# Kernel optimization log

Measured on AMD Instinct MI355X. Metric: run time of the kernel, lower is better.

## Reference

```python
import jax, jax.numpy as jnp
import numpy as np

B, R, C, IC, OC = 32, 16384, 16, 16, 16  # batch, num_routes, num_capsules, in_ch, out_ch
NUM_ITERATIONS = 3


def squash(s, axis=-1):
    # scale * s / norm with scale = norm^2/(1+norm^2)  ==  norm/(1+norm^2) * s
    norm = jnp.linalg.norm(s, axis=axis, keepdims=True)
    return (norm / (1.0 + norm * norm)) * s


def setup_inputs() -> dict:
    key = jax.random.key(0)
    kx, kw = jax.random.split(key)
    x = jax.random.normal(kx, (B, C, IC), dtype=jnp.float32)
    # W param: torch shape (1, R, C, OC, IC); leading 1 squeezed here
    W = jax.random.normal(kw, (R, C, OC, IC), dtype=jnp.float32)
    return {"x": x, "W": W}


def reference(x, W):
    # u_hat[b,r,c,o] = sum_i W[r,c,o,i] * x[b,c,i]   (torch broadcast of x over routes)
    u_hat = jnp.einsum('rcoi,bci->brco', W, x)  # (B, R, C, OC)
    b = jnp.zeros((x.shape[0], R, C, 1), dtype=u_hat.dtype)
    outputs = None
    for it in range(NUM_ITERATIONS):
        c = jax.nn.softmax(b, axis=1)                      # softmax over routes
        s = (c * u_hat).sum(axis=1, keepdims=True)         # (B, 1, C, OC)
        outputs = squash(s)
        if it < NUM_ITERATIONS - 1:
            b = b + (u_hat * outputs).sum(axis=-1, keepdims=True)
    return outputs.squeeze(axis=1)  # (B, C, OC)
```

## Files before the change

### kernel.cpp

```cpp
#include <hip/hip_runtime.h>
#include <math.h>


typedef __attribute__((ext_vector_type(8)))  short short8;
typedef __attribute__((ext_vector_type(16))) float f32x16;

union FU { short8 s; unsigned int u[4]; };

typedef const __attribute__((address_space(1))) void GV;
typedef __attribute__((address_space(3))) void LV;

__device__ __forceinline__ void splitpk(float a, float b,
                                        unsigned int& hp, unsigned int& lp) {
    unsigned int ua = __float_as_uint(a), ub = __float_as_uint(b);
    unsigned int ta = ua + 0x7FFFu + ((ua >> 16) & 1u);
    unsigned int tb = ub + 0x7FFFu + ((ub >> 16) & 1u);
    hp = (ta >> 16) | (tb & 0xFFFF0000u);
    float ha = __uint_as_float(ta & 0xFFFF0000u);
    float hb = __uint_as_float(tb & 0xFFFF0000u);
    unsigned int la = __float_as_uint(a - ha) + 0x8000u;
    unsigned int lb = __float_as_uint(b - hb) + 0x8000u;
    lp = (la >> 16) | (lb & 0xFFFF0000u);
}

__global__ __launch_bounds__(256) void k_zero(float* __restrict__ ws) {
    ws[blockIdx.x * 256 + threadIdx.x] = 0.f;
}

__global__ __launch_bounds__(256) void k_wsum(const float4* __restrict__ W4,
                                              float* __restrict__ wsum) {
    int gid = blockIdx.x * 256 + threadIdx.x;
    float4 acc = {0.f, 0.f, 0.f, 0.f};
    int idx = gid;
    #pragma unroll
    for (int it = 0; it < 64; ++it) {
        float4 w = W4[idx];
        acc.x += w.x; acc.y += w.y; acc.z += w.z; acc.w += w.w;
        idx += 262144;
    }
    int cls = gid & 1023;
    atomicAdd(&wsum[cls * 4 + 0], acc.x);
    atomicAdd(&wsum[cls * 4 + 1], acc.y);
    atomicAdd(&wsum[cls * 4 + 2], acc.z);
    atomicAdd(&wsum[cls * 4 + 3], acc.w);
}

__global__ __launch_bounds__(256) void k_v1(const float* __restrict__ wsum,
                                            const float* __restrict__ x,
                                            float* __restrict__ v1) {
    int t = blockIdx.x * 256 + threadIdx.x;
    int o = t & 15, c = (t >> 4) & 15, b = t >> 8;
    const float* xb = x + (b * 16 + c) * 16;
    const float* wr = wsum + (c * 16 + o) * 16;
    float s = 0.f;
    #pragma unroll
    for (int i = 0; i < 16; ++i) s += wr[i] * xb[i];
    s *= (1.0f / 16384.0f);
    float ns = s * s;
    #pragma unroll
    for (int d = 1; d < 16; d <<= 1) ns += __shfl_xor(ns, d);
    v1[t] = s * (sqrtf(ns) / (1.0f + ns));
}

__global__ __launch_bounds__(256) void k_vout_vs(const float* __restrict__ E,
                                                 const float* __restrict__ Z,
                                                 const float* __restrict__ v1,
                                                 float* __restrict__ vs) {
    int t = blockIdx.x * 256 + threadIdx.x;
    float s = E[t] / Z[t >> 4];
    float ns = s * s;
    #pragma unroll
    for (int d = 1; d < 16; d <<= 1) ns += __shfl_xor(ns, d);
    vs[t] = v1[t] + s * (sqrtf(ns) / (1.0f + ns));
}

__global__ __launch_bounds__(256) void k_vout(const float* __restrict__ E,
                                              const float* __restrict__ Z,
                                              float* __restrict__ dst) {
    int t = blockIdx.x * 256 + threadIdx.x;
    float s = E[t] / Z[t >> 4];
    float ns = s * s;
    #pragma unroll
    for (int d = 1; d < 16; d <<= 1) ns += __shfl_xor(ns, d);
    dst[t] = s * (sqrtf(ns) / (1.0f + ns));
}

__global__ __launch_bounds__(512)
void k_iter(const float* __restrict__ W,
            const float* __restrict__ x,
            const float* __restrict__ v,
            float* __restrict__ E,
            float* __restrict__ Z) {
    __shared__ float4 Wr[4 * 1024];
    __shared__ float sV[512];
    __shared__ float E_lds[512];
    __shared__ float Z_lds[32];

    int c = blockIdx.y;
    int r0 = blockIdx.x * 256;
    int tid = threadIdx.x, wv = tid >> 6, l = tid & 63;
    int m  = l & 31;
    int hi = l >> 5;

    { int b = tid >> 4, o = tid & 15;
      sV[tid] = v[b * 256 + c * 16 + o];
      E_lds[tid] = 0.f; }
    if (tid < 32) Z_lds[tid] = 0.f;

    FU bh, bl;
    {
        const float4* xb = (const float4*)x + m * 64 + c * 4 + hi * 2;
        float4 x0 = xb[0], x1 = xb[1];
        splitpk(x0.x, x0.y, bh.u[0], bl.u[0]);
        splitpk(x0.z, x0.w, bh.u[1], bl.u[1]);
        splitpk(x1.x, x1.y, bh.u[2], bl.u[2]);
        splitpk(x1.z, x1.w, bh.u[3], bl.u[3]);
    }
    __syncthreads();

    float vf[16];
    #pragma unroll
    for (int reg = 0; reg < 16; ++reg) {
        int o = (reg & 3) + 4 * hi + 8 * ((reg >> 2) & 1);
        vf[reg] = sV[m * 16 + o];
    }

    float accE[16];
    #pragma unroll
    for (int reg = 0; reg < 16; ++reg) accE[reg] = 0.f;
    float accZ = 0.f;

    asm volatile("s_waitcnt vmcnt(0)" ::: "memory");

    const float4* W4c = (const float4*)W + (size_t)c * 64;

#define STAGE(sl, cn) {                                                        \
        const float4* s0 = W4c +                                               \
            (size_t)(r0 + (cn) * 16 + wv * 2 + (m >> 4)) * 1024 +              \
            (m & 15) * 4 + hi * 2;                                             \
        __builtin_amdgcn_global_load_lds((GV*)s0,                              \
            (LV*)&Wr[(sl) * 1024 + wv * 128], 16, 0, 0);                       \
        __builtin_amdgcn_global_load_lds((GV*)(s0 + 1),                        \
            (LV*)&Wr[(sl) * 1024 + wv * 128 + 64], 16, 0, 0);                  \
    }

    STAGE(0, 0); STAGE(1, 1); STAGE(2, 2);

    #pragma unroll
    for (int chunk = 0; chunk < 16; ++chunk) {
        if (chunk <= 12) STAGE((chunk + 3) & 3, chunk + 3);

        if (chunk <= 12)      asm volatile("s_waitcnt vmcnt(6)" ::: "memory");
        else if (chunk == 13) asm volatile("s_waitcnt vmcnt(4)" ::: "memory");
        else if (chunk == 14) asm volatile("s_waitcnt vmcnt(2)" ::: "memory");
        else                  asm volatile("s_waitcnt vmcnt(0)" ::: "memory");

        int sb = (chunk & 3) * 1024 + wv * 128 + l;
        float4 ca = Wr[sb];
        float4 cb = Wr[sb + 64];

        FU ah, al;
        splitpk(ca.x, ca.y, ah.u[0], al.u[0]);
        splitpk(ca.z, ca.w, ah.u[1], al.u[1]);
        splitpk(cb.x, cb.y, ah.u[2], al.u[2]);
        splitpk(cb.z, cb.w, ah.u[3], al.u[3]);

        f32x16 cf;
        #pragma unroll
        for (int i = 0; i < 16; ++i) cf[i] = 0.f;
        cf = __builtin_amdgcn_mfma_f32_32x32x16_bf16(al.s, bl.s, cf, 0, 0, 0);
        cf = __builtin_amdgcn_mfma_f32_32x32x16_bf16(ah.s, bl.s, cf, 0, 0, 0);
        cf = __builtin_amdgcn_mfma_f32_32x32x16_bf16(al.s, bh.s, cf, 0, 0, 0);
        cf = __builtin_amdgcn_mfma_f32_32x32x16_bf16(ah.s, bh.s, cf, 0, 0, 0);

        float Lp0 = 0.f, Lp1 = 0.f;
        #pragma unroll
        for (int reg = 0; reg < 8; ++reg)  Lp0 += cf[reg] * vf[reg];
        #pragma unroll
        for (int reg = 8; reg < 16; ++reg) Lp1 += cf[reg] * vf[reg];
        float Lv0 = Lp0 + __shfl_xor(Lp0, 32);
        float Lv1 = Lp1 + __shfl_xor(Lp1, 32);
        float e0 = __expf(Lv0), e1 = __expf(Lv1);
        accZ += e0 + e1;
        #pragma unroll
        for (int reg = 0; reg < 8; ++reg)  accE[reg] += e0 * cf[reg];
        #pragma unroll
        for (int reg = 8; reg < 16; ++reg) accE[reg] += e1 * cf[reg];
    }
#undef STAGE

    #pragma unroll
    for (int j = 0; j < 8; ++j) {
        int o = (j & 3) + 4 * hi + 8 * (j >> 2);
        atomicAdd(&E_lds[m * 16 + o], accE[j] + accE[j + 8]);
    }
    if (l < 32) atomicAdd(&Z_lds[m], accZ);
    __syncthreads();

    atomicAdd(&E[(tid >> 4) * 256 + c * 16 + (tid & 15)], E_lds[tid]);
    if (tid < 32) atomicAdd(&Z[tid * 16 + c], Z_lds[tid]);
}

extern "C" void kernel_launch(void* const* d_in, const int* in_sizes, int n_in,
                              void* d_out, int out_size, void* d_ws, size_t ws_size,
                              hipStream_t stream) {
    const float* x = (const float*)d_in[0];
    const float* W = (const float*)d_in[1];
    float* out = (float*)d_out;
    float* ws = (float*)d_ws;

    float* wsum = ws + 0;
    float* E2   = ws + 4096;
    float* Z2   = ws + 12288;
    float* E3   = ws + 12800;
    float* Z3   = ws + 20992;
    float* v1   = ws + 21504;
    float* vs   = ws + 29696;

    k_zero<<<84, 256, 0, stream>>>(ws);

    k_wsum<<<1024, 256, 0, stream>>>((const float4*)W, wsum);
    k_v1<<<32, 256, 0, stream>>>(wsum, x, v1);

    k_iter<<<dim3(64, 16), 512, 0, stream>>>(W, x, v1, E2, Z2);
    k_vout_vs<<<32, 256, 0, stream>>>(E2, Z2, v1, vs);

    k_iter<<<dim3(64, 16), 512, 0, stream>>>(W, x, vs, E3, Z3);
    k_vout<<<32, 256, 0, stream>>>(E3, Z3, out);
}
```

Baseline: 204.2 us.

## Remap k_iter so each wave owns a capsule and blocks span contiguous routes

```diff
diff --git a/kernel.cpp b/kernel.cpp
--- a/kernel.cpp
+++ b/kernel.cpp
@@ -92,20 +92,12 @@
             float* __restrict__ E,
             float* __restrict__ Z) {
     __shared__ float4 Wr[4 * 1024];
-    __shared__ float sV[512];
-    __shared__ float E_lds[512];
-    __shared__ float Z_lds[32];
-
-    int c = blockIdx.y;
-    int r0 = blockIdx.x * 256;
+
     int tid = threadIdx.x, wv = tid >> 6, l = tid & 63;
     int m  = l & 31;
     int hi = l >> 5;
-
-    { int b = tid >> 4, o = tid & 15;
-      sV[tid] = v[b * 256 + c * 16 + o];
-      E_lds[tid] = 0.f; }
-    if (tid < 32) Z_lds[tid] = 0.f;
+    int c  = blockIdx.y * 8 + wv;
+    int r0 = blockIdx.x * 64;
 
     FU bh, bl;
     {
@@ -116,13 +108,12 @@
         splitpk(x1.x, x1.y, bh.u[2], bl.u[2]);
         splitpk(x1.z, x1.w, bh.u[3], bl.u[3]);
     }
-    __syncthreads();
 
     float vf[16];
     #pragma unroll
     for (int reg = 0; reg < 16; ++reg) {
         int o = (reg & 3) + 4 * hi + 8 * ((reg >> 2) & 1);
-        vf[reg] = sV[m * 16 + o];
+        vf[reg] = v[m * 256 + c * 16 + o];
     }
 
     float accE[16];
@@ -132,29 +123,18 @@
 
     asm volatile("s_waitcnt vmcnt(0)" ::: "memory");
 
-    const float4* W4c = (const float4*)W + (size_t)c * 64;
+    const float4* Wsrc = (const float4*)W +
+        ((size_t)(r0 + (m >> 4)) * 1024 + c * 64 + (m & 15) * 4 + hi * 2);
 
 #define STAGE(sl, cn) {                                                        \
-        const float4* s0 = W4c +                                               \
-            (size_t)(r0 + (cn) * 16 + wv * 2 + (m >> 4)) * 1024 +              \
-            (m & 15) * 4 + hi * 2;                                             \
+        const float4* s0 = Wsrc + (size_t)(cn) * 2048;                         \
         __builtin_amdgcn_global_load_lds((GV*)s0,                              \
             (LV*)&Wr[(sl) * 1024 + wv * 128], 16, 0, 0);                       \
         __builtin_amdgcn_global_load_lds((GV*)(s0 + 1),                        \
             (LV*)&Wr[(sl) * 1024 + wv * 128 + 64], 16, 0, 0);                  \
     }
 
-    STAGE(0, 0); STAGE(1, 1); STAGE(2, 2);
-
-    #pragma unroll
-    for (int chunk = 0; chunk < 16; ++chunk) {
-        if (chunk <= 12) STAGE((chunk + 3) & 3, chunk + 3);
-
-        if (chunk <= 12)      asm volatile("s_waitcnt vmcnt(6)" ::: "memory");
-        else if (chunk == 13) asm volatile("s_waitcnt vmcnt(4)" ::: "memory");
-        else if (chunk == 14) asm volatile("s_waitcnt vmcnt(2)" ::: "memory");
-        else                  asm volatile("s_waitcnt vmcnt(0)" ::: "memory");
-
+    auto body = [&](int chunk) {
         int sb = (chunk & 3) * 1024 + wv * 128 + l;
         float4 ca = Wr[sb];
         float4 cb = Wr[sb + 64];
@@ -186,19 +166,27 @@
         for (int reg = 0; reg < 8; ++reg)  accE[reg] += e0 * cf[reg];
         #pragma unroll
         for (int reg = 8; reg < 16; ++reg) accE[reg] += e1 * cf[reg];
-    }
+    };
+
+    STAGE(0, 0); STAGE(1, 1); STAGE(2, 2);
+
+    #pragma unroll 2
+    for (int chunk = 0; chunk < 29; ++chunk) {
+        STAGE((chunk + 3) & 3, chunk + 3);
+        asm volatile("s_waitcnt vmcnt(6)" ::: "memory");
+        body(chunk);
+    }
+    asm volatile("s_waitcnt vmcnt(4)" ::: "memory"); body(29);
+    asm volatile("s_waitcnt vmcnt(2)" ::: "memory"); body(30);
+    asm volatile("s_waitcnt vmcnt(0)" ::: "memory"); body(31);
 #undef STAGE
 
     #pragma unroll
     for (int j = 0; j < 8; ++j) {
         int o = (j & 3) + 4 * hi + 8 * (j >> 2);
-        atomicAdd(&E_lds[m * 16 + o], accE[j] + accE[j + 8]);
-    }
-    if (l < 32) atomicAdd(&Z_lds[m], accZ);
-    __syncthreads();
-
-    atomicAdd(&E[(tid >> 4) * 256 + c * 16 + (tid & 15)], E_lds[tid]);
-    if (tid < 32) atomicAdd(&Z[tid * 16 + c], Z_lds[tid]);
+        atomicAdd(&E[m * 256 + c * 16 + o], accE[j] + accE[j + 8]);
+    }
+    if (l < 32) atomicAdd(&Z[m * 16 + c], accZ);
 }
 
 extern "C" void kernel_launch(void* const* d_in, const int* in_sizes, int n_in,
@@ -222,9 +210,9 @@
     k_wsum<<<1024, 256, 0, stream>>>((const float4*)W, wsum);
     k_v1<<<32, 256, 0, stream>>>(wsum, x, v1);
 
-    k_iter<<<dim3(64, 16), 512, 0, stream>>>(W, x, v1, E2, Z2);
+    k_iter<<<dim3(256, 2), 512, 0, stream>>>(W, x, v1, E2, Z2);
     k_vout_vs<<<32, 256, 0, stream>>>(E2, Z2, v1, vs);
 
-    k_iter<<<dim3(64, 16), 512, 0, stream>>>(W, x, vs, E3, Z3);
+    k_iter<<<dim3(256, 2), 512, 0, stream>>>(W, x, vs, E3, Z3);
     k_vout<<<32, 256, 0, stream>>>(E3, Z3, out);
 }
```

Measured after the change: 511.1 us. +150.3%, slower.
